# Performance work log

Hardware: AMD Instinct MI355X
Metric: run time of the kernel (lower is better)

The kernel has to match this reference:

```python
import jax, jax.numpy as jnp
import numpy as np

G, S, D, H, E = 8, 2048, 1024, 4096, 8  # groups, group_size, d_model, ffn_hidden, experts


def setup_inputs() -> dict:
    key = jax.random.key(0)
    ks = jax.random.split(key, 6)
    s = 0.02
    return {
        "x": jax.random.normal(ks[0], (G, S, D), dtype=jnp.float32),
        "gate_w": jax.random.normal(ks[1], (D, E), dtype=jnp.float32) * s,
        "ew1": jax.random.normal(ks[2], (E, D, H), dtype=jnp.float32) * s,
        "eb1": jnp.zeros((E, H), dtype=jnp.float32),
        "ew2": jax.random.normal(ks[3], (E, H, D), dtype=jnp.float32) * s,
        "eb2": jnp.zeros((E, D), dtype=jnp.float32),
        "sw1": jax.random.normal(ks[4], (D, H), dtype=jnp.float32) * s,
        "sb1": jnp.zeros((H,), dtype=jnp.float32),
        "sw2": jax.random.normal(ks[5], (H, D), dtype=jnp.float32) * s,
        "sb2": jnp.zeros((D,), dtype=jnp.float32),
        "expert_capacity": 2048,
    }


def reference(x, gate_w, ew1, eb1, ew2, eb2, sw1, sb1, sw2, sb2, expert_capacity):
    g, s_, d = x.shape
    e = gate_w.shape[1]
    T = g * s_
    cap = int(expert_capacity)

    # ---- Router (inference path) ----
    router_logits = jnp.einsum('gsd,de->gse', x, gate_w)           # (G,S,E)
    router_probs = jax.nn.softmax(router_logits, axis=-1)
    flat_probs = router_probs.transpose(2, 0, 1).reshape(e, T)      # (E,T)
    pad_w = max(0, cap - T)
    if pad_w > 0:
        flat_probs = jnp.pad(flat_probs, ((0, 0), (0, pad_w)),
                             mode='constant', constant_values=-1e9)
    scores, token_indices = jax.lax.top_k(flat_probs, k=cap)        # (E,C)
    scores = jnp.where(scores > -1e8, scores, 0.0)

    # ---- Routed experts: gather -> grouped FFN -> scale -> scatter-add ----
    x_flat = x.reshape(T, d)                                        # (T,D)
    safe_idx = jnp.clip(token_indices, 0, T - 1)                    # guard padded slots
    toks = x_flat[safe_idx]                                         # (E,C,D)
    h = jax.nn.gelu(jnp.einsum('ecd,edh->ech', toks, ew1) + eb1[:, None, :])
    y = jnp.einsum('ech,ehd->ecd', h, ew2) + eb2[:, None, :]        # (E,C,D)
    y = y * scores[..., None]                                       # zero weight kills padded slots
    routed = jnp.zeros_like(x_flat).at[safe_idx.reshape(-1)].add(y.reshape(-1, d))

    # ---- Shared expert over all tokens ----
    shared = jax.nn.gelu(x_flat @ sw1 + sb1) @ sw2 + sb2            # (T,D)

    return (routed + shared).reshape(g, s_, d)
```

## Files before the change

### kernel.cpp

```cpp
#include <hip/hip_runtime.h>

typedef __bf16 bf16;
typedef __bf16 bf16x8 __attribute__((ext_vector_type(8)));
typedef float f32x4 __attribute__((ext_vector_type(4)));

#define NTOK 16384
#define DMODEL 1024
#define HFFN 4096
#define NEXP 8
#define CAP 2048

#define VMCNT(n) asm volatile("s_waitcnt vmcnt(" #n ")" ::: "memory")
#define LGKM0() do { asm volatile("s_waitcnt lgkmcnt(0)" ::: "memory"); \
                     __builtin_amdgcn_sched_barrier(0); } while (0)
#define RAWBAR() do { __builtin_amdgcn_sched_barrier(0); \
                      __builtin_amdgcn_s_barrier(); \
                      __builtin_amdgcn_sched_barrier(0); } while (0)

__device__ __forceinline__ void gload16(const void* g, void* l) {
  __builtin_amdgcn_global_load_lds((const __attribute__((address_space(1))) void*)g,
                                   (__attribute__((address_space(3))) void*)l, 16, 0, 0);
}

__device__ __forceinline__ float gelu_f(float v) {
  float u = 0.7978845608028654f * (v + 0.044715f * v * v * v);
  float ex = __expf(2.0f * u);
  float th = 1.0f - 2.0f / (ex + 1.0f);
  return 0.5f * v * (1.0f + th);
}

__device__ __forceinline__ void xcd_remap(int& bx, int& by) {
  const int gx = gridDim.x;
  const int lg = 31 - __clz((unsigned)gx);
  const int w = blockIdx.x + gx * blockIdx.y;
  bx = (w >> 3) & (gx - 1);
  by = (w & 7) | (((w >> 3) >> lg) << 3);
}

__global__ __launch_bounds__(256) void cvt_x_kernel(const float* __restrict__ x,
                                                    bf16* __restrict__ xb) {
  int i = blockIdx.x * blockDim.x + threadIdx.x;
  const float4* a = (const float4*)x + (size_t)i * 2;
  float4 v0 = a[0], v1 = a[1];
  bf16x8 o;
  o[0]=(bf16)v0.x; o[1]=(bf16)v0.y; o[2]=(bf16)v0.z; o[3]=(bf16)v0.w;
  o[4]=(bf16)v1.x; o[5]=(bf16)v1.y; o[6]=(bf16)v1.z; o[7]=(bf16)v1.w;
  *(bf16x8*)(xb + (size_t)i * 8) = o;
}

__global__ __launch_bounds__(64) void router_kernel(const float* __restrict__ x,
                                                    const float* __restrict__ gw,
                                                    float* __restrict__ probs) {
  int t = blockIdx.x;
  int l = threadIdx.x;
  int e = l & 7, chunk = l >> 3;
  const float* xr = x + (size_t)t * DMODEL + chunk * 128;
  const float* gwr = gw + (size_t)(chunk * 128) * NEXP + e;
  float a0 = 0.f, a1 = 0.f;
  #pragma unroll
  for (int d = 0; d < 128; d += 8) {
    float4 xv = *(const float4*)(xr + d);
    float4 xw = *(const float4*)(xr + d + 4);
    a0 += xv.x * gwr[(d+0)*8] + xv.y * gwr[(d+1)*8] + xv.z * gwr[(d+2)*8] + xv.w * gwr[(d+3)*8];
    a1 += xw.x * gwr[(d+4)*8] + xw.y * gwr[(d+5)*8] + xw.z * gwr[(d+6)*8] + xw.w * gwr[(d+7)*8];
  }
  float acc = a0 + a1;
  acc += __shfl_xor(acc, 8);
  acc += __shfl_xor(acc, 16);
  acc += __shfl_xor(acc, 32);
  float m = acc;
  m = fmaxf(m, __shfl_xor(m, 1));
  m = fmaxf(m, __shfl_xor(m, 2));
  m = fmaxf(m, __shfl_xor(m, 4));
  float ex = expf(acc - m);
  float s = ex;
  s += __shfl_xor(s, 1); s += __shfl_xor(s, 2); s += __shfl_xor(s, 4);
  if (l < 8) probs[(size_t)e * NTOK + t] = ex / s;
}

__global__ __launch_bounds__(256) void topk_kernel(const float* __restrict__ probs,
                                                   int* __restrict__ oidx,
                                                   float* __restrict__ oscr) {
  const int e = blockIdx.x;
  const float* p = probs + (size_t)e * NTOK;
  const int t = threadIdx.x;
  __shared__ unsigned hist[256];
  __shared__ unsigned sg[256], sq[256];
  __shared__ unsigned bcast[4];
  unsigned pref = 0, krem = CAP;
  for (int pass = 0; pass < 4; ++pass) {
    const int sh = 24 - pass * 8;
    hist[t] = 0;
    __syncthreads();
    for (int j = 0; j < 64; ++j) {
      unsigned u = __float_as_uint(p[t * 64 + j]);
      bool ok = (pass == 0) || ((u >> (sh + 8)) == pref);
      if (ok) atomicAdd(&hist[(u >> sh) & 255u], 1u);
    }
    __syncthreads();
    if (t == 0) {
      unsigned cum = 0; int b = 255;
      for (; b > 0; --b) {
        unsigned c = hist[b];
        if (cum + c >= krem) break;
        cum += c;
      }
      bcast[0] = (pref << 8) | (unsigned)b;
      bcast[1] = krem - cum;
    }
    __syncthreads();
    pref = bcast[0];
    krem = bcast[1];
  }
  const unsigned thr = pref;
  const unsigned neq_take = krem;
  unsigned cgt = 0, ceq = 0;
  for (int j = 0; j < 64; ++j) {
    unsigned u = __float_as_uint(p[t * 64 + j]);
    cgt += (u > thr);
    ceq += (u == thr);
  }
  sg[t] = cgt; sq[t] = ceq;
  __syncthreads();
  if (t == 0) {
    unsigned ag = 0, aq = 0;
    for (int i = 0; i < 256; ++i) {
      unsigned g = sg[i], q = sq[i];
      sg[i] = ag; sq[i] = aq;
      ag += g; aq += q;
    }
    bcast[2] = ag;
  }
  __syncthreads();
  const unsigned ngt = bcast[2];
  unsigned og = sg[t], oq = sq[t];
  int* oi = oidx + e * CAP;
  float* os = oscr + e * CAP;
  for (int j = 0; j < 64; ++j) {
    int tok = t * 64 + j;
    float pv = p[tok];
    unsigned u = __float_as_uint(pv);
    if (u > thr) {
      oi[og] = tok; os[og] = pv; ++og;
    } else if (u == thr) {
      if (oq < neq_take) { oi[ngt + oq] = tok; os[ngt + oq] = pv; }
      ++oq;
    }
  }
}

__global__ __launch_bounds__(256) void transpose_cvt(const float* __restrict__ in_e,
                                                     const float* __restrict__ in_s,
                                                     bf16* __restrict__ outp,
                                                     int R, int C) {
  int z = blockIdx.z;
  const float* in = (z < 8) ? (in_e + (size_t)z * (size_t)R * C) : in_s;
  bf16* out = outp + (size_t)z * (size_t)R * C;
  __shared__ float tile[64][65];
  int tx = threadIdx.x & 63, ty = threadIdx.x >> 6;
  int c0 = blockIdx.x * 64, r0 = blockIdx.y * 64;
  #pragma unroll
  for (int j = 0; j < 16; ++j) {
    int r = ty + j * 4;
    tile[r][tx] = in[(size_t)(r0 + r) * C + c0 + tx];
  }
  __syncthreads();
  #pragma unroll
  for (int j = 0; j < 16; ++j) {
    int c = ty + j * 4;
    out[(size_t)(c0 + c) * R + r0 + tx] = (bf16)tile[tx][c];
  }
}


#define STAGE(t, bb) do { \
  bf16* S_ = smem + (bb) * 16384; \
  const int ko_ = (t) * 32; \
  gload16(srcA0 + ko_, S_ + ldst); \
  gload16(srcA1 + ko_, S_ + 4096 + ldst); \
  gload16(srcB0 + ko_, S_ + 8192 + ldst); \
  gload16(srcB1 + ko_, S_ + 12288 + ldst); \
} while (0)

#define MFMA_BLK(ILO, JLO) \
  _Pragma("unroll") \
  for (int i = 0; i < 4; ++i) \
    _Pragma("unroll") \
    for (int j = 0; j < 2; ++j) \
      acc[(ILO) + i][(JLO) + j] = __builtin_amdgcn_mfma_f32_16x16x32_bf16( \
          (ILO) ? avh[i] : avl[i], bv[(JLO) + j], acc[(ILO) + i][(JLO) + j], 0, 0, 0)

#define KLOOP(NT) do { \
  STAGE(0, 0); \
  STAGE(1, 1); \
  VMCNT(4); \
  RAWBAR(); \
  int b = 0; \
  for (int t = 0; t < (NT); ++t) { \
    int b2 = b + 2; if (b2 >= 3) b2 -= 3; \
    const bool st = (t + 2 < (NT)); \
    bf16* S2 = smem + b2 * 16384; \
    const int ko2 = (t + 2) * 32; \
    const bf16* As = smem + b * 16384; \
    const bf16* Bs = As + 8192; \
    bf16x8 avl[4], avh[4], bv[4]; \
     \
    _Pragma("unroll") \
    for (int i = 0; i < 4; ++i) \
      avl[i] = *(const bf16x8*)(As + (wr * 128 + i * 16 + fr) * 32 + fch); \
    bv[0] = *(const bf16x8*)(Bs + (wc * 64 + fr) * 32 + fch); \
    bv[1] = *(const bf16x8*)(Bs + (wc * 64 + 16 + fr) * 32 + fch); \
    if (st) gload16(srcA0 + ko2, S2 + ldst); \
    RAWBAR(); LGKM0(); \
    __builtin_amdgcn_s_setprio(1); MFMA_BLK(0, 0); __builtin_amdgcn_s_setprio(0); \
    RAWBAR(); \
     \
    bv[2] = *(const bf16x8*)(Bs + (wc * 64 + 32 + fr) * 32 + fch); \
    bv[3] = *(const bf16x8*)(Bs + (wc * 64 + 48 + fr) * 32 + fch); \
    if (st) gload16(srcA1 + ko2, S2 + 4096 + ldst); \
    RAWBAR(); LGKM0(); \
    __builtin_amdgcn_s_setprio(1); MFMA_BLK(0, 2); __builtin_amdgcn_s_setprio(0); \
    RAWBAR(); \
     \
    _Pragma("unroll") \
    for (int i = 0; i < 4; ++i) \
      avh[i] = *(const bf16x8*)(As + (wr * 128 + 64 + i * 16 + fr) * 32 + fch); \
    if (st) gload16(srcB0 + ko2, S2 + 8192 + ldst); \
    RAWBAR(); LGKM0(); \
    __builtin_amdgcn_s_setprio(1); MFMA_BLK(4, 0); __builtin_amdgcn_s_setprio(0); \
    RAWBAR(); \
     \
    if (st) gload16(srcB1 + ko2, S2 + 12288 + ldst); \
    __builtin_amdgcn_s_setprio(1); MFMA_BLK(4, 2); __builtin_amdgcn_s_setprio(0); \
    if (st) { VMCNT(4); } else { VMCNT(0); } \
    RAWBAR(); \
    if (++b == 3) b = 0; \
  } \
} while (0)

__global__ __launch_bounds__(512, 2) void ffn1_gemm(const bf16* __restrict__ xb,
                                                    const bf16* __restrict__ w1t,
                                                    const float* __restrict__ bias1,
                                                    const int* __restrict__ sel,
                                                    bf16* __restrict__ hout,
                                                    int routed) {
  const int e = blockIdx.z;
  const bf16* Bw = w1t + (routed ? (size_t)e * HFFN * DMODEL : 0);
  const float* bias = bias1 + (routed ? (size_t)e * HFFN : 0);
  bf16* hb = hout + (routed ? (size_t)e * CAP * HFFN : 0);
  int bx, by;
  xcd_remap(bx, by);
  const int m0 = by * 256, n0 = bx * 256;
  __shared__ __align__(16) bf16 smem[49152];
  const int tid = threadIdx.x, lane = tid & 63, wave = tid >> 6;
  const int wr = wave >> 2, wc = wave & 3;

  const int srow = tid >> 2, sch = tid & 3;
  const int schs = sch ^ ((srow >> 1) & 3);
  const int ldst = srow * 32 + sch * 8;
  const bf16 *srcA0, *srcA1, *srcB0, *srcB1;
  {
    int r0i = routed ? sel[e * CAP + m0 + srow] : (m0 + srow);
    int r1i = routed ? sel[e * CAP + m0 + 128 + srow] : (m0 + 128 + srow);
    srcA0 = xb + (size_t)r0i * DMODEL + schs * 8;
    srcA1 = xb + (size_t)r1i * DMODEL + schs * 8;
    srcB0 = Bw + (size_t)(n0 + srow) * DMODEL + schs * 8;
    srcB1 = Bw + (size_t)(n0 + 128 + srow) * DMODEL + schs * 8;
  }

  f32x4 acc[8][4];
  #pragma unroll
  for (int i = 0; i < 8; ++i)
    #pragma unroll
    for (int j = 0; j < 4; ++j) acc[i][j] = (f32x4){0.f, 0.f, 0.f, 0.f};

  const int fr = lane & 15;
  const int fch = ((lane >> 4) ^ ((lane >> 1) & 3)) * 8;

  KLOOP(DMODEL / 32);

  #pragma unroll
  for (int half = 0; half < 2; ++half) {
    if (wr == half) {
      #pragma unroll
      for (int i = 0; i < 8; ++i) {
        #pragma unroll
        for (int j = 0; j < 4; ++j) {
          const int nl = wc * 64 + j * 16 + fr;
          const float bb = bias[n0 + nl];
          #pragma unroll
          for (int q = 0; q < 4; ++q) {
            const int ml = i * 16 + (lane >> 4) * 4 + q;
            smem[ml * 256 + (nl ^ (((ml >> 2) & 7) << 4))] =
                (bf16)gelu_f(acc[i][j][q] + bb);
          }
        }
      }
    }
    __syncthreads();
    #pragma unroll
    for (int p = 0; p < 8; ++p) {
      const int flat = p * 512 + tid;
      const int row = flat >> 5, nc8 = flat & 31;
      uint4 v = *(const uint4*)(smem + row * 256 + ((nc8 * 8) ^ (((row >> 2) & 7) << 4)));
      *(uint4*)(hb + (size_t)(m0 + half * 128 + row) * HFFN + n0 + nc8 * 8) = v;
    }
    __syncthreads();
  }
}

__global__ __launch_bounds__(512, 2) void ffn2_gemm(const bf16* __restrict__ hbuf,
                                                    const bf16* __restrict__ w2t,
                                                    const float* __restrict__ bias2,
                                                    const int* __restrict__ sel,
                                                    const float* __restrict__ scr,
                                                    float* __restrict__ out,
                                                    int routed) {
  const int e = blockIdx.z;
  const bf16* Ab = hbuf + (routed ? (size_t)e * CAP * HFFN : 0);
  const bf16* Bw = w2t + (routed ? (size_t)e * DMODEL * HFFN : 0);
  const float* bias = bias2 + (routed ? (size_t)e * DMODEL : 0);
  int bx, by;
  xcd_remap(bx, by);
  const int m0 = by * 256, n0 = bx * 256;
  __shared__ __align__(16) bf16 smem[49152];
  __shared__ int s_tok[256];
  __shared__ float s_scl[256];
  const int tid = threadIdx.x, lane = tid & 63, wave = tid >> 6;
  const int wr = wave >> 2, wc = wave & 3;

  const int srow = tid >> 2, sch = tid & 3;
  const int schs = sch ^ ((srow >> 1) & 3);
  const int ldst = srow * 32 + sch * 8;
  const bf16* srcA0 = Ab + (size_t)(m0 + srow) * HFFN + schs * 8;
  const bf16* srcA1 = Ab + (size_t)(m0 + 128 + srow) * HFFN + schs * 8;
  const bf16* srcB0 = Bw + (size_t)(n0 + srow) * HFFN + schs * 8;
  const bf16* srcB1 = Bw + (size_t)(n0 + 128 + srow) * HFFN + schs * 8;
  if (routed && tid < 256) {
    s_tok[tid] = sel[e * CAP + m0 + tid];
    s_scl[tid] = scr[e * CAP + m0 + tid];
  }

  f32x4 acc[8][4];
  #pragma unroll
  for (int i = 0; i < 8; ++i)
    #pragma unroll
    for (int j = 0; j < 4; ++j) acc[i][j] = (f32x4){0.f, 0.f, 0.f, 0.f};

  const int fr = lane & 15;
  const int fch = ((lane >> 4) ^ ((lane >> 1) & 3)) * 8;

  KLOOP(HFFN / 32);

  if (!routed) {
    #pragma unroll
    for (int i = 0; i < 8; ++i) {
      #pragma unroll
      for (int j = 0; j < 4; ++j) {
        const int nl = wc * 64 + j * 16 + fr;
        const float bb = bias[n0 + nl];
        #pragma unroll
        for (int q = 0; q < 4; ++q) {
          const int ml = wr * 128 + i * 16 + (lane >> 4) * 4 + q;
          out[(size_t)(m0 + ml) * DMODEL + n0 + nl] = acc[i][j][q] + bb;
        }
      }
    }
  } else {
    __syncthreads();
    #pragma unroll
    for (int i = 0; i < 8; ++i) {
      #pragma unroll
      for (int j = 0; j < 4; ++j) {
        const int nl = wc * 64 + j * 16 + fr;
        const float bb = bias[n0 + nl];
        #pragma unroll
        for (int q = 0; q < 4; ++q) {
          const int ml = wr * 128 + i * 16 + (lane >> 4) * 4 + q;
          const int tok = s_tok[ml];
          const float sc = s_scl[ml];
          atomicAdd(out + (size_t)tok * DMODEL + n0 + nl, (acc[i][j][q] + bb) * sc);
        }
      }
    }
  }
}

extern "C" void kernel_launch(void* const* d_in, const int* in_sizes, int n_in,
                              void* d_out, int out_size, void* d_ws, size_t ws_size,
                              hipStream_t stream) {
  const float* x   = (const float*)d_in[0];
  const float* gw  = (const float*)d_in[1];
  const float* ew1 = (const float*)d_in[2];
  const float* eb1 = (const float*)d_in[3];
  const float* ew2 = (const float*)d_in[4];
  const float* eb2 = (const float*)d_in[5];
  const float* sw1 = (const float*)d_in[6];
  const float* sb1 = (const float*)d_in[7];
  const float* sw2 = (const float*)d_in[8];
  const float* sb2 = (const float*)d_in[9];
  float* out = (float*)d_out;

  char* ws = (char*)d_ws;
  size_t off = 0;
  bf16* xb      = (bf16*)(ws + off); off += (size_t)NTOK * DMODEL * 2;
  bf16* w1t     = (bf16*)(ws + off); off += (size_t)9 * HFFN * DMODEL * 2;
  bf16* w2t     = (bf16*)(ws + off); off += (size_t)9 * DMODEL * HFFN * 2;
  bf16* hbuf    = (bf16*)(ws + off); off += (size_t)NTOK * HFFN * 2;
  float* probs  = (float*)(ws + off); off += (size_t)NEXP * NTOK * 4;
  int* selidx   = (int*)(ws + off);   off += (size_t)NEXP * CAP * 4;
  float* selscr = (float*)(ws + off); off += (size_t)NEXP * CAP * 4;

  cvt_x_kernel<<<dim3(NTOK * DMODEL / 8 / 256), dim3(256), 0, stream>>>(x, xb);
  router_kernel<<<dim3(NTOK), dim3(64), 0, stream>>>(x, gw, probs);
  topk_kernel<<<dim3(NEXP), dim3(256), 0, stream>>>(probs, selidx, selscr);
  transpose_cvt<<<dim3(HFFN / 64, DMODEL / 64, 9), dim3(256), 0, stream>>>(ew1, sw1, w1t, DMODEL, HFFN);
  transpose_cvt<<<dim3(DMODEL / 64, HFFN / 64, 9), dim3(256), 0, stream>>>(ew2, sw2, w2t, HFFN, DMODEL);

  ffn1_gemm<<<dim3(HFFN / 256, NTOK / 256, 1), dim3(512), 0, stream>>>(
      xb, w1t + (size_t)8 * HFFN * DMODEL, sb1, (const int*)nullptr, hbuf, 0);
  ffn2_gemm<<<dim3(DMODEL / 256, NTOK / 256, 1), dim3(512), 0, stream>>>(
      hbuf, w2t + (size_t)8 * DMODEL * HFFN, sb2, (const int*)nullptr, (const float*)nullptr, out, 0);

  ffn1_gemm<<<dim3(HFFN / 256, CAP / 256, NEXP), dim3(512), 0, stream>>>(
      xb, w1t, eb1, selidx, hbuf, 1);
  ffn2_gemm<<<dim3(DMODEL / 256, CAP / 256, NEXP), dim3(512), 0, stream>>>(
      hbuf, w2t, eb2, selidx, selscr, out, 1);
}
```

Measured before the change: 976.8 us.

## Switch GEMM K-loop to BK=64 double-buffered tiles with 8-way swizzle

Replaces the triple-buffered BK=32 K-loop with a double-buffered BK=64 loop, halving the number of iterations and barriers per K extent. LDS grows to 128 KB per block and the swizzle pattern changes to an 8-chunk XOR. Prefetch of tile t+2 is written into the buffer being consumed this iteration, split across the MFMA phases. The larger LDS footprint likely limits occupancy to one block per CU despite launch_bounds(512,2). There is also a possible race: the buffer is refilled while later phases still read it.

```diff
diff --git a/kernel.cpp b/kernel.cpp
--- a/kernel.cpp
+++ b/kernel.cpp
@@ -173,68 +173,101 @@
 }
 
 
-#define STAGE(t, bb) do { \
-  bf16* S_ = smem + (bb) * 16384; \
-  const int ko_ = (t) * 32; \
-  gload16(srcA0 + ko_, S_ + ldst); \
-  gload16(srcA1 + ko_, S_ + 4096 + ldst); \
-  gload16(srcB0 + ko_, S_ + 8192 + ldst); \
-  gload16(srcB1 + ko_, S_ + 12288 + ldst); \
+#define STAGE_TILE_ALL(tt) do { \
+  bf16* D_ = smem + (((tt) & 1) << 15); \
+  const int ko_ = (tt) * 64; \
+  gload16(srcA0 + ko_, D_ + tid8); \
+  gload16(srcA1 + ko_, D_ + 4096 + tid8); \
+  gload16(srcA2 + ko_, D_ + 8192 + tid8); \
+  gload16(srcA3 + ko_, D_ + 12288 + tid8); \
+  gload16(srcB0 + ko_, D_ + 16384 + tid8); \
+  gload16(srcB1 + ko_, D_ + 20480 + tid8); \
+  gload16(srcB2 + ko_, D_ + 24576 + tid8); \
+  gload16(srcB3 + ko_, D_ + 28672 + tid8); \
 } while (0)
 
-#define MFMA_BLK(ILO, JLO) \
-  _Pragma("unroll") \
-  for (int i = 0; i < 4; ++i) \
-    _Pragma("unroll") \
-    for (int j = 0; j < 2; ++j) \
-      acc[(ILO) + i][(JLO) + j] = __builtin_amdgcn_mfma_f32_16x16x32_bf16( \
-          (ILO) ? avh[i] : avl[i], bv[(JLO) + j], acc[(ILO) + i][(JLO) + j], 0, 0, 0)
-
-#define KLOOP(NT) do { \
-  STAGE(0, 0); \
-  STAGE(1, 1); \
-  VMCNT(4); \
+#define KLOOP8(NT) do { \
+  STAGE_TILE_ALL(0); \
+  STAGE_TILE_ALL(1); \
+  VMCNT(8); \
   RAWBAR(); \
-  int b = 0; \
   for (int t = 0; t < (NT); ++t) { \
-    int b2 = b + 2; if (b2 >= 3) b2 -= 3; \
-    const bool st = (t + 2 < (NT)); \
-    bf16* S2 = smem + b2 * 16384; \
-    const int ko2 = (t + 2) * 32; \
-    const bf16* As = smem + b * 16384; \
-    const bf16* Bs = As + 8192; \
-    bf16x8 avl[4], avh[4], bv[4]; \
+    const bf16* Ab_ = smem + ((t & 1) << 15); \
+    const bf16* Bb_ = Ab_ + 16384; \
+    bf16* Sn_ = smem + ((t & 1) << 15); \
+    const int ko2 = (t + 2) * 64; \
+    const bool st = (t + 2) < (NT); \
+    bf16x8 aA[8], aB[8]; \
      \
-    _Pragma("unroll") \
-    for (int i = 0; i < 4; ++i) \
-      avl[i] = *(const bf16x8*)(As + (wr * 128 + i * 16 + fr) * 32 + fch); \
-    bv[0] = *(const bf16x8*)(Bs + (wc * 64 + fr) * 32 + fch); \
-    bv[1] = *(const bf16x8*)(Bs + (wc * 64 + 16 + fr) * 32 + fch); \
-    if (st) gload16(srcA0 + ko2, S2 + ldst); \
+    _Pragma("unroll") for (int i = 0; i < 4; ++i) { \
+      aA[i*2+0] = *(const bf16x8*)(Ab_ + (wr*128 + i*16 + fr)*64 + c0s); \
+      aA[i*2+1] = *(const bf16x8*)(Ab_ + (wr*128 + i*16 + fr)*64 + c1s); \
+    } \
+    _Pragma("unroll") for (int j = 0; j < 2; ++j) { \
+      aB[j*2+0] = *(const bf16x8*)(Bb_ + (wc*64 + j*16 + fr)*64 + c0s); \
+      aB[j*2+1] = *(const bf16x8*)(Bb_ + (wc*64 + j*16 + fr)*64 + c1s); \
+    } \
     RAWBAR(); LGKM0(); \
-    __builtin_amdgcn_s_setprio(1); MFMA_BLK(0, 0); __builtin_amdgcn_s_setprio(0); \
+    __builtin_amdgcn_s_setprio(1); \
+    _Pragma("unroll") for (int i = 0; i < 4; ++i) \
+      _Pragma("unroll") for (int j = 0; j < 2; ++j) { \
+        acc[i][j] = __builtin_amdgcn_mfma_f32_16x16x32_bf16(aA[i*2+0], aB[j*2+0], acc[i][j], 0, 0, 0); \
+        acc[i][j] = __builtin_amdgcn_mfma_f32_16x16x32_bf16(aA[i*2+1], aB[j*2+1], acc[i][j], 0, 0, 0); \
+      } \
+    __builtin_amdgcn_s_setprio(0); \
     RAWBAR(); \
      \
-    bv[2] = *(const bf16x8*)(Bs + (wc * 64 + 32 + fr) * 32 + fch); \
-    bv[3] = *(const bf16x8*)(Bs + (wc * 64 + 48 + fr) * 32 + fch); \
-    if (st) gload16(srcA1 + ko2, S2 + 4096 + ldst); \
+    _Pragma("unroll") for (int j = 0; j < 2; ++j) { \
+      aB[4+j*2+0] = *(const bf16x8*)(Bb_ + (wc*64 + 32 + j*16 + fr)*64 + c0s); \
+      aB[4+j*2+1] = *(const bf16x8*)(Bb_ + (wc*64 + 32 + j*16 + fr)*64 + c1s); \
+    } \
+    if (st) { \
+      gload16(srcA0 + ko2, Sn_ + tid8); \
+      gload16(srcA2 + ko2, Sn_ + 8192 + tid8); \
+    } \
     RAWBAR(); LGKM0(); \
-    __builtin_amdgcn_s_setprio(1); MFMA_BLK(0, 2); __builtin_amdgcn_s_setprio(0); \
+    __builtin_amdgcn_s_setprio(1); \
+    _Pragma("unroll") for (int i = 0; i < 4; ++i) \
+      _Pragma("unroll") for (int j = 0; j < 2; ++j) { \
+        acc[i][2+j] = __builtin_amdgcn_mfma_f32_16x16x32_bf16(aA[i*2+0], aB[4+j*2+0], acc[i][2+j], 0, 0, 0); \
+        acc[i][2+j] = __builtin_amdgcn_mfma_f32_16x16x32_bf16(aA[i*2+1], aB[4+j*2+1], acc[i][2+j], 0, 0, 0); \
+      } \
+    __builtin_amdgcn_s_setprio(0); \
     RAWBAR(); \
      \
-    _Pragma("unroll") \
-    for (int i = 0; i < 4; ++i) \
-      avh[i] = *(const bf16x8*)(As + (wr * 128 + 64 + i * 16 + fr) * 32 + fch); \
-    if (st) gload16(srcB0 + ko2, S2 + 8192 + ldst); \
+    _Pragma("unroll") for (int i = 0; i < 4; ++i) { \
+      aA[i*2+0] = *(const bf16x8*)(Ab_ + (wr*128 + 64 + i*16 + fr)*64 + c0s); \
+      aA[i*2+1] = *(const bf16x8*)(Ab_ + (wr*128 + 64 + i*16 + fr)*64 + c1s); \
+    } \
+    if (st) { \
+      gload16(srcB0 + ko2, Sn_ + 16384 + tid8); \
+      gload16(srcB1 + ko2, Sn_ + 20480 + tid8); \
+      gload16(srcB2 + ko2, Sn_ + 24576 + tid8); \
+      gload16(srcB3 + ko2, Sn_ + 28672 + tid8); \
+    } \
     RAWBAR(); LGKM0(); \
-    __builtin_amdgcn_s_setprio(1); MFMA_BLK(4, 0); __builtin_amdgcn_s_setprio(0); \
+    __builtin_amdgcn_s_setprio(1); \
+    _Pragma("unroll") for (int i = 0; i < 4; ++i) \
+      _Pragma("unroll") for (int j = 0; j < 2; ++j) { \
+        acc[4+i][j] = __builtin_amdgcn_mfma_f32_16x16x32_bf16(aA[i*2+0], aB[j*2+0], acc[4+i][j], 0, 0, 0); \
+        acc[4+i][j] = __builtin_amdgcn_mfma_f32_16x16x32_bf16(aA[i*2+1], aB[j*2+1], acc[4+i][j], 0, 0, 0); \
+      } \
+    __builtin_amdgcn_s_setprio(0); \
     RAWBAR(); \
      \
-    if (st) gload16(srcB1 + ko2, S2 + 12288 + ldst); \
-    __builtin_amdgcn_s_setprio(1); MFMA_BLK(4, 2); __builtin_amdgcn_s_setprio(0); \
-    if (st) { VMCNT(4); } else { VMCNT(0); } \
+    if (st) { \
+      gload16(srcA1 + ko2, Sn_ + 4096 + tid8); \
+      gload16(srcA3 + ko2, Sn_ + 12288 + tid8); \
+    } \
+    __builtin_amdgcn_s_setprio(1); \
+    _Pragma("unroll") for (int i = 0; i < 4; ++i) \
+      _Pragma("unroll") for (int j = 0; j < 2; ++j) { \
+        acc[4+i][2+j] = __builtin_amdgcn_mfma_f32_16x16x32_bf16(aA[i*2+0], aB[4+j*2+0], acc[4+i][2+j], 0, 0, 0); \
+        acc[4+i][2+j] = __builtin_amdgcn_mfma_f32_16x16x32_bf16(aA[i*2+1], aB[4+j*2+1], acc[4+i][2+j], 0, 0, 0); \
+      } \
+    __builtin_amdgcn_s_setprio(0); \
+    if (st) { VMCNT(8); } else { VMCNT(0); } \
     RAWBAR(); \
-    if (++b == 3) b = 0; \
   } \
 } while (0)
 
@@ -251,21 +284,27 @@
   int bx, by;
   xcd_remap(bx, by);
   const int m0 = by * 256, n0 = bx * 256;
-  __shared__ __align__(16) bf16 smem[49152];
+  __shared__ __align__(16) bf16 smem[65536];
   const int tid = threadIdx.x, lane = tid & 63, wave = tid >> 6;
   const int wr = wave >> 2, wc = wave & 3;
-
-  const int srow = tid >> 2, sch = tid & 3;
-  const int schs = sch ^ ((srow >> 1) & 3);
-  const int ldst = srow * 32 + sch * 8;
-  const bf16 *srcA0, *srcA1, *srcB0, *srcB1;
+  const int tid8 = tid * 8;
+
+  const int srow = tid >> 3, sch = tid & 7;
+  const int schs = sch ^ (srow & 7);
+  const bf16 *srcA0, *srcA1, *srcA2, *srcA3, *srcB0, *srcB1, *srcB2, *srcB3;
   {
-    int r0i = routed ? sel[e * CAP + m0 + srow] : (m0 + srow);
-    int r1i = routed ? sel[e * CAP + m0 + 128 + srow] : (m0 + 128 + srow);
-    srcA0 = xb + (size_t)r0i * DMODEL + schs * 8;
-    srcA1 = xb + (size_t)r1i * DMODEL + schs * 8;
+    int ra0 = routed ? sel[e * CAP + m0 + srow]       : (m0 + srow);
+    int ra1 = routed ? sel[e * CAP + m0 + 64 + srow]  : (m0 + 64 + srow);
+    int ra2 = routed ? sel[e * CAP + m0 + 128 + srow] : (m0 + 128 + srow);
+    int ra3 = routed ? sel[e * CAP + m0 + 192 + srow] : (m0 + 192 + srow);
+    srcA0 = xb + (size_t)ra0 * DMODEL + schs * 8;
+    srcA1 = xb + (size_t)ra1 * DMODEL + schs * 8;
+    srcA2 = xb + (size_t)ra2 * DMODEL + schs * 8;
+    srcA3 = xb + (size_t)ra3 * DMODEL + schs * 8;
     srcB0 = Bw + (size_t)(n0 + srow) * DMODEL + schs * 8;
-    srcB1 = Bw + (size_t)(n0 + 128 + srow) * DMODEL + schs * 8;
+    srcB1 = Bw + (size_t)(n0 + 64 + srow) * DMODEL + schs * 8;
+    srcB2 = Bw + (size_t)(n0 + 128 + srow) * DMODEL + schs * 8;
+    srcB3 = Bw + (size_t)(n0 + 192 + srow) * DMODEL + schs * 8;
   }
 
   f32x4 acc[8][4];
@@ -275,9 +314,12 @@
     for (int j = 0; j < 4; ++j) acc[i][j] = (f32x4){0.f, 0.f, 0.f, 0.f};
 
   const int fr = lane & 15;
-  const int fch = ((lane >> 4) ^ ((lane >> 1) & 3)) * 8;
-
-  KLOOP(DMODEL / 32);
+  const int k8 = lane >> 4;
+  const int sw = lane & 7;
+  const int c0s = (k8 ^ sw) * 8;
+  const int c1s = ((k8 + 4) ^ sw) * 8;
+
+  KLOOP8(DMODEL / 64);
 
   #pragma unroll
   for (int half = 0; half < 2; ++half) {
@@ -323,19 +365,23 @@
   int bx, by;
   xcd_remap(bx, by);
   const int m0 = by * 256, n0 = bx * 256;
-  __shared__ __align__(16) bf16 smem[49152];
+  __shared__ __align__(16) bf16 smem[65536];
   __shared__ int s_tok[256];
   __shared__ float s_scl[256];
   const int tid = threadIdx.x, lane = tid & 63, wave = tid >> 6;
   const int wr = wave >> 2, wc = wave & 3;
-
-  const int srow = tid >> 2, sch = tid & 3;
-  const int schs = sch ^ ((srow >> 1) & 3);
-  const int ldst = srow * 32 + sch * 8;
+  const int tid8 = tid * 8;
+
+  const int srow = tid >> 3, sch = tid & 7;
+  const int schs = sch ^ (srow & 7);
   const bf16* srcA0 = Ab + (size_t)(m0 + srow) * HFFN + schs * 8;
-  const bf16* srcA1 = Ab + (size_t)(m0 + 128 + srow) * HFFN + schs * 8;
+  const bf16* srcA1 = Ab + (size_t)(m0 + 64 + srow) * HFFN + schs * 8;
+  const bf16* srcA2 = Ab + (size_t)(m0 + 128 + srow) * HFFN + schs * 8;
+  const bf16* srcA3 = Ab + (size_t)(m0 + 192 + srow) * HFFN + schs * 8;
   const bf16* srcB0 = Bw + (size_t)(n0 + srow) * HFFN + schs * 8;
-  const bf16* srcB1 = Bw + (size_t)(n0 + 128 + srow) * HFFN + schs * 8;
+  const bf16* srcB1 = Bw + (size_t)(n0 + 64 + srow) * HFFN + schs * 8;
+  const bf16* srcB2 = Bw + (size_t)(n0 + 128 + srow) * HFFN + schs * 8;
+  const bf16* srcB3 = Bw + (size_t)(n0 + 192 + srow) * HFFN + schs * 8;
   if (routed && tid < 256) {
     s_tok[tid] = sel[e * CAP + m0 + tid];
     s_scl[tid] = scr[e * CAP + m0 + tid];
@@ -348,9 +394,12 @@
     for (int j = 0; j < 4; ++j) acc[i][j] = (f32x4){0.f, 0.f, 0.f, 0.f};
 
   const int fr = lane & 15;
-  const int fch = ((lane >> 4) ^ ((lane >> 1) & 3)) * 8;
-
-  KLOOP(HFFN / 32);
+  const int k8 = lane >> 4;
+  const int sw = lane & 7;
+  const int c0s = (k8 ^ sw) * 8;
+  const int c1s = ((k8 + 4) ^ sw) * 8;
+
+  KLOOP8(HFFN / 64);
 
   if (!routed) {
     #pragma unroll
```

Result: faster. 897.2 us (-8.1%).

## Shrink GEMM tiles to 128x256 with double-buffered K loop and faster GELU

Applied to the files above, without the earlier changes.

The FFN GEMMs move from 256x256 tiles with a triple-buffered, finely interleaved K loop to 128x256 tiles with a simpler double-buffered loop. They now use half the LDS and a smaller accumulator, and launch bounds are raised to four blocks per SM. GELU is rewritten as a sigmoid form using exp2 and a hardware reciprocal. The aim is higher occupancy and less barrier overhead, at the cost of more A/B reloads per FLOP and a full vmcnt(0) wait each iteration that serialises load and compute.

```diff
diff --git a/kernel.cpp b/kernel.cpp
--- a/kernel.cpp
+++ b/kernel.cpp
@@ -10,12 +10,10 @@
 #define NEXP 8
 #define CAP 2048
 
-#define VMCNT(n) asm volatile("s_waitcnt vmcnt(" #n ")" ::: "memory")
-#define LGKM0() do { asm volatile("s_waitcnt lgkmcnt(0)" ::: "memory"); \
-                     __builtin_amdgcn_sched_barrier(0); } while (0)
-#define RAWBAR() do { __builtin_amdgcn_sched_barrier(0); \
-                      __builtin_amdgcn_s_barrier(); \
-                      __builtin_amdgcn_sched_barrier(0); } while (0)
+#define VMCNT0() asm volatile("s_waitcnt vmcnt(0)" ::: "memory")
+#define BARRIER() __builtin_amdgcn_s_barrier()
+#define PRIO1() __builtin_amdgcn_s_setprio(1)
+#define PRIO0() __builtin_amdgcn_s_setprio(0)
 
 __device__ __forceinline__ void gload16(const void* g, void* l) {
   __builtin_amdgcn_global_load_lds((const __attribute__((address_space(1))) void*)g,
@@ -23,10 +21,10 @@
 }
 
 __device__ __forceinline__ float gelu_f(float v) {
-  float u = 0.7978845608028654f * (v + 0.044715f * v * v * v);
-  float ex = __expf(2.0f * u);
-  float th = 1.0f - 2.0f / (ex + 1.0f);
-  return 0.5f * v * (1.0f + th);
+  float t = v * v;
+  float s2 = v * fmaf(0.10294358f, t, 2.3022084f);
+  float e = __builtin_exp2f(-s2);
+  return v * __builtin_amdgcn_rcpf(1.0f + e);
 }
 
 __device__ __forceinline__ void xcd_remap(int& bx, int& by) {
@@ -173,72 +171,44 @@
 }
 
 
-#define STAGE(t, bb) do { \
-  bf16* S_ = smem + (bb) * 16384; \
-  const int ko_ = (t) * 32; \
-  gload16(srcA0 + ko_, S_ + ldst); \
-  gload16(srcA1 + ko_, S_ + 4096 + ldst); \
-  gload16(srcB0 + ko_, S_ + 8192 + ldst); \
-  gload16(srcB1 + ko_, S_ + 12288 + ldst); \
-} while (0)
-
-#define MFMA_BLK(ILO, JLO) \
-  _Pragma("unroll") \
-  for (int i = 0; i < 4; ++i) \
-    _Pragma("unroll") \
-    for (int j = 0; j < 2; ++j) \
-      acc[(ILO) + i][(JLO) + j] = __builtin_amdgcn_mfma_f32_16x16x32_bf16( \
-          (ILO) ? avh[i] : avl[i], bv[(JLO) + j], acc[(ILO) + i][(JLO) + j], 0, 0, 0)
-
-#define KLOOP(NT) do { \
-  STAGE(0, 0); \
-  STAGE(1, 1); \
-  VMCNT(4); \
-  RAWBAR(); \
-  int b = 0; \
+#define KLOOP(NT, STRIDE) do { \
+  {  \
+    bf16* D_ = smem; \
+    gload16(srcA0, D_ + tid8); \
+    gload16(srcB0, D_ + 4096 + tid8); \
+    gload16(srcB1, D_ + 8192 + tid8); \
+    VMCNT0(); \
+    BARRIER(); \
+  } \
   for (int t = 0; t < (NT); ++t) { \
-    int b2 = b + 2; if (b2 >= 3) b2 -= 3; \
-    const bool st = (t + 2 < (NT)); \
-    bf16* S2 = smem + b2 * 16384; \
-    const int ko2 = (t + 2) * 32; \
-    const bf16* As = smem + b * 16384; \
-    const bf16* Bs = As + 8192; \
-    bf16x8 avl[4], avh[4], bv[4]; \
-     \
-    _Pragma("unroll") \
-    for (int i = 0; i < 4; ++i) \
-      avl[i] = *(const bf16x8*)(As + (wr * 128 + i * 16 + fr) * 32 + fch); \
-    bv[0] = *(const bf16x8*)(Bs + (wc * 64 + fr) * 32 + fch); \
-    bv[1] = *(const bf16x8*)(Bs + (wc * 64 + 16 + fr) * 32 + fch); \
-    if (st) gload16(srcA0 + ko2, S2 + ldst); \
-    RAWBAR(); LGKM0(); \
-    __builtin_amdgcn_s_setprio(1); MFMA_BLK(0, 0); __builtin_amdgcn_s_setprio(0); \
-    RAWBAR(); \
-     \
-    bv[2] = *(const bf16x8*)(Bs + (wc * 64 + 32 + fr) * 32 + fch); \
-    bv[3] = *(const bf16x8*)(Bs + (wc * 64 + 48 + fr) * 32 + fch); \
-    if (st) gload16(srcA1 + ko2, S2 + 4096 + ldst); \
-    RAWBAR(); LGKM0(); \
-    __builtin_amdgcn_s_setprio(1); MFMA_BLK(0, 2); __builtin_amdgcn_s_setprio(0); \
-    RAWBAR(); \
-     \
-    _Pragma("unroll") \
-    for (int i = 0; i < 4; ++i) \
-      avh[i] = *(const bf16x8*)(As + (wr * 128 + 64 + i * 16 + fr) * 32 + fch); \
-    if (st) gload16(srcB0 + ko2, S2 + 8192 + ldst); \
-    RAWBAR(); LGKM0(); \
-    __builtin_amdgcn_s_setprio(1); MFMA_BLK(4, 0); __builtin_amdgcn_s_setprio(0); \
-    RAWBAR(); \
-     \
-    if (st) gload16(srcB1 + ko2, S2 + 12288 + ldst); \
-    __builtin_amdgcn_s_setprio(1); MFMA_BLK(4, 2); __builtin_amdgcn_s_setprio(0); \
-    if (st) { VMCNT(4); } else { VMCNT(0); } \
-    RAWBAR(); \
-    if (++b == 3) b = 0; \
+    const bf16* buf = smem + (t & 1) * 12288; \
+    bf16x8 aA[4], aB[4]; \
+    _Pragma("unroll") for (int i = 0; i < 4; ++i) { \
+      const int ra = wr * 64 + i * 16 + fr; \
+      aA[i] = *(const bf16x8*)(buf + ra * 32 + ((k4 ^ ((ra >> 1) & 3)) << 3)); \
+    } \
+    _Pragma("unroll") for (int j = 0; j < 4; ++j) { \
+      const int rb = wc * 64 + j * 16 + fr; \
+      aB[j] = *(const bf16x8*)(buf + 4096 + rb * 32 + ((k4 ^ ((rb >> 1) & 3)) << 3)); \
+    } \
+    if (t + 1 < (NT)) { \
+      bf16* D_ = smem + ((t + 1) & 1) * 12288; \
+      const int ko = (t + 1) * 32; \
+      gload16(srcA0 + ko, D_ + tid8); \
+      gload16(srcB0 + ko, D_ + 4096 + tid8); \
+      gload16(srcB1 + ko, D_ + 8192 + tid8); \
+    } \
+    PRIO1(); \
+    _Pragma("unroll") for (int i = 0; i < 4; ++i) \
+      _Pragma("unroll") for (int j = 0; j < 4; ++j) \
+        acc[i][j] = __builtin_amdgcn_mfma_f32_16x16x32_bf16(aA[i], aB[j], acc[i][j], 0, 0, 0); \
+    PRIO0(); \
+    VMCNT0(); \
+    BARRIER(); \
   } \
 } while (0)
 
-__global__ __launch_bounds__(512, 2) void ffn1_gemm(const bf16* __restrict__ xb,
+__global__ __launch_bounds__(512, 4) void ffn1_gemm(const bf16* __restrict__ xb,
                                                     const bf16* __restrict__ w1t,
                                                     const float* __restrict__ bias1,
                                                     const int* __restrict__ sel,
@@ -250,48 +220,45 @@
   bf16* hb = hout + (routed ? (size_t)e * CAP * HFFN : 0);
   int bx, by;
   xcd_remap(bx, by);
-  const int m0 = by * 256, n0 = bx * 256;
-  __shared__ __align__(16) bf16 smem[49152];
+  const int m0 = by * 128, n0 = bx * 256;
+  __shared__ __align__(16) bf16 smem[24576];
   const int tid = threadIdx.x, lane = tid & 63, wave = tid >> 6;
   const int wr = wave >> 2, wc = wave & 3;
+  const int tid8 = tid * 8;
+  const int fr = lane & 15, k4 = lane >> 4;
 
   const int srow = tid >> 2, sch = tid & 3;
   const int schs = sch ^ ((srow >> 1) & 3);
-  const int ldst = srow * 32 + sch * 8;
-  const bf16 *srcA0, *srcA1, *srcB0, *srcB1;
+  const bf16 *srcA0, *srcB0, *srcB1;
   {
-    int r0i = routed ? sel[e * CAP + m0 + srow] : (m0 + srow);
-    int r1i = routed ? sel[e * CAP + m0 + 128 + srow] : (m0 + 128 + srow);
-    srcA0 = xb + (size_t)r0i * DMODEL + schs * 8;
-    srcA1 = xb + (size_t)r1i * DMODEL + schs * 8;
+    int ra = routed ? sel[e * CAP + m0 + srow] : (m0 + srow);
+    srcA0 = xb + (size_t)ra * DMODEL + schs * 8;
     srcB0 = Bw + (size_t)(n0 + srow) * DMODEL + schs * 8;
     srcB1 = Bw + (size_t)(n0 + 128 + srow) * DMODEL + schs * 8;
   }
 
-  f32x4 acc[8][4];
-  #pragma unroll
-  for (int i = 0; i < 8; ++i)
+  f32x4 acc[4][4];
+  #pragma unroll
+  for (int i = 0; i < 4; ++i)
     #pragma unroll
     for (int j = 0; j < 4; ++j) acc[i][j] = (f32x4){0.f, 0.f, 0.f, 0.f};
 
-  const int fr = lane & 15;
-  const int fch = ((lane >> 4) ^ ((lane >> 1) & 3)) * 8;
-
-  KLOOP(DMODEL / 32);
-
+  KLOOP(DMODEL / 32, DMODEL);
+
+  __syncthreads();
   #pragma unroll
   for (int half = 0; half < 2; ++half) {
-    if (wr == half) {
+    if ((wc >> 1) == half) {
       #pragma unroll
-      for (int i = 0; i < 8; ++i) {
+      for (int i = 0; i < 4; ++i) {
         #pragma unroll
         for (int j = 0; j < 4; ++j) {
-          const int nl = wc * 64 + j * 16 + fr;
-          const float bb = bias[n0 + nl];
+          const int cl = (wc & 1) * 64 + j * 16 + fr;
+          const float bb = bias[n0 + half * 128 + cl];
           #pragma unroll
           for (int q = 0; q < 4; ++q) {
-            const int ml = i * 16 + (lane >> 4) * 4 + q;
-            smem[ml * 256 + (nl ^ (((ml >> 2) & 7) << 4))] =
+            const int ml = wr * 64 + i * 16 + k4 * 4 + q;
+            smem[ml * 128 + (cl ^ (((ml >> 2) & 7) << 4))] =
                 (bf16)gelu_f(acc[i][j][q] + bb);
           }
         }
@@ -299,17 +266,17 @@
     }
     __syncthreads();
     #pragma unroll
-    for (int p = 0; p < 8; ++p) {
-      const int flat = p * 512 + tid;
-      const int row = flat >> 5, nc8 = flat & 31;
-      uint4 v = *(const uint4*)(smem + row * 256 + ((nc8 * 8) ^ (((row >> 2) & 7) << 4)));
-      *(uint4*)(hb + (size_t)(m0 + half * 128 + row) * HFFN + n0 + nc8 * 8) = v;
-    }
-    __syncthreads();
-  }
-}
-
-__global__ __launch_bounds__(512, 2) void ffn2_gemm(const bf16* __restrict__ hbuf,
+    for (int p = 0; p < 4; ++p) {
+      const int f = p * 512 + tid;
+      const int row = f >> 4, c8 = f & 15;
+      uint4 v = *(const uint4*)(smem + row * 128 + ((c8 * 8) ^ (((row >> 2) & 7) << 4)));
+      *(uint4*)(hb + (size_t)(m0 + row) * HFFN + n0 + half * 128 + c8 * 8) = v;
+    }
+    __syncthreads();
+  }
+}
+
+__global__ __launch_bounds__(512, 4) void ffn2_gemm(const bf16* __restrict__ hbuf,
                                                     const bf16* __restrict__ w2t,
                                                     const float* __restrict__ bias2,
                                                     const int* __restrict__ sel,
@@ -322,46 +289,43 @@
   const float* bias = bias2 + (routed ? (size_t)e * DMODEL : 0);
   int bx, by;
   xcd_remap(bx, by);
-  const int m0 = by * 256, n0 = bx * 256;
-  __shared__ __align__(16) bf16 smem[49152];
-  __shared__ int s_tok[256];
-  __shared__ float s_scl[256];
+  const int m0 = by * 128, n0 = bx * 256;
+  __shared__ __align__(16) bf16 smem[24576];
+  __shared__ int s_tok[128];
+  __shared__ float s_scl[128];
   const int tid = threadIdx.x, lane = tid & 63, wave = tid >> 6;
   const int wr = wave >> 2, wc = wave & 3;
+  const int tid8 = tid * 8;
+  const int fr = lane & 15, k4 = lane >> 4;
 
   const int srow = tid >> 2, sch = tid & 3;
   const int schs = sch ^ ((srow >> 1) & 3);
-  const int ldst = srow * 32 + sch * 8;
   const bf16* srcA0 = Ab + (size_t)(m0 + srow) * HFFN + schs * 8;
-  const bf16* srcA1 = Ab + (size_t)(m0 + 128 + srow) * HFFN + schs * 8;
   const bf16* srcB0 = Bw + (size_t)(n0 + srow) * HFFN + schs * 8;
   const bf16* srcB1 = Bw + (size_t)(n0 + 128 + srow) * HFFN + schs * 8;
-  if (routed && tid < 256) {
+  if (routed && tid < 128) {
     s_tok[tid] = sel[e * CAP + m0 + tid];
     s_scl[tid] = scr[e * CAP + m0 + tid];
   }
 
-  f32x4 acc[8][4];
-  #pragma unroll
-  for (int i = 0; i < 8; ++i)
+  f32x4 acc[4][4];
+  #pragma unroll
+  for (int i = 0; i < 4; ++i)
     #pragma unroll
     for (int j = 0; j < 4; ++j) acc[i][j] = (f32x4){0.f, 0.f, 0.f, 0.f};
 
-  const int fr = lane & 15;
-  const int fch = ((lane >> 4) ^ ((lane >> 1) & 3)) * 8;
-
-  KLOOP(HFFN / 32);
+  KLOOP(HFFN / 32, HFFN);
 
   if (!routed) {
     #pragma unroll
-    for (int i = 0; i < 8; ++i) {
+    for (int i = 0; i < 4; ++i) {
       #pragma unroll
       for (int j = 0; j < 4; ++j) {
         const int nl = wc * 64 + j * 16 + fr;
         const float bb = bias[n0 + nl];
         #pragma unroll
         for (int q = 0; q < 4; ++q) {
-          const int ml = wr * 128 + i * 16 + (lane >> 4) * 4 + q;
+          const int ml = wr * 64 + i * 16 + k4 * 4 + q;
           out[(size_t)(m0 + ml) * DMODEL + n0 + nl] = acc[i][j][q] + bb;
         }
       }
@@ -369,14 +333,14 @@
   } else {
     __syncthreads();
     #pragma unroll
-    for (int i = 0; i < 8; ++i) {
+    for (int i = 0; i < 4; ++i) {
       #pragma unroll
       for (int j = 0; j < 4; ++j) {
         const int nl = wc * 64 + j * 16 + fr;
         const float bb = bias[n0 + nl];
         #pragma unroll
         for (int q = 0; q < 4; ++q) {
-          const int ml = wr * 128 + i * 16 + (lane >> 4) * 4 + q;
+          const int ml = wr * 64 + i * 16 + k4 * 4 + q;
           const int tok = s_tok[ml];
           const float sc = s_scl[ml];
           atomicAdd(out + (size_t)tok * DMODEL + n0 + nl, (acc[i][j][q] + bb) * sc);
@@ -417,13 +381,13 @@
   transpose_cvt<<<dim3(HFFN / 64, DMODEL / 64, 9), dim3(256), 0, stream>>>(ew1, sw1, w1t, DMODEL, HFFN);
   transpose_cvt<<<dim3(DMODEL / 64, HFFN / 64, 9), dim3(256), 0, stream>>>(ew2, sw2, w2t, HFFN, DMODEL);
 
-  ffn1_gemm<<<dim3(HFFN / 256, NTOK / 256, 1), dim3(512), 0, stream>>>(
+  ffn1_gemm<<<dim3(HFFN / 256, NTOK / 128, 1), dim3(512), 0, stream>>>(
       xb, w1t + (size_t)8 * HFFN * DMODEL, sb1, (const int*)nullptr, hbuf, 0);
-  ffn2_gemm<<<dim3(DMODEL / 256, NTOK / 256, 1), dim3(512), 0, stream>>>(
+  ffn2_gemm<<<dim3(DMODEL / 256, NTOK / 128, 1), dim3(512), 0, stream>>>(
       hbuf, w2t + (size_t)8 * DMODEL * HFFN, sb2, (const int*)nullptr, (const float*)nullptr, out, 0);
 
-  ffn1_gemm<<<dim3(HFFN / 256, CAP / 256, NEXP), dim3(512), 0, stream>>>(
+  ffn1_gemm<<<dim3(HFFN / 256, CAP / 128, NEXP), dim3(512), 0, stream>>>(
       xb, w1t, eb1, selidx, hbuf, 1);
-  ffn2_gemm<<<dim3(DMODEL / 256, CAP / 256, NEXP), dim3(512), 0, stream>>>(
+  ffn2_gemm<<<dim3(DMODEL / 256, CAP / 128, NEXP), dim3(512), 0, stream>>>(
       hbuf, w2t, eb2, selidx, selscr, out, 1);
 }
```

Measured after the change: 917.5 us. 1.06x faster.
